# Kernel tuning notes

Measured on AMD Instinct MI355X. Metric: run time of the kernel, lower is better.

The kernel has to match this reference:

```python
import jax, jax.numpy as jnp
import numpy as np

B, L, D = 8, 2048, 64
EPS = 1e-8


def setup_inputs() -> dict:
    key = jax.random.key(0)
    ks = jax.random.split(key, 7)
    s = 1.0 / np.sqrt(D)  # ~ torch Linear default init scale
    return {
        "x": jax.random.normal(ks[0], (B, L, D), dtype=jnp.float32),
        "B_w": jax.random.normal(ks[1], (D, D), dtype=jnp.float32) * s,
        "B_b": jax.random.normal(ks[2], (D,), dtype=jnp.float32) * s,
        "C_w": jax.random.normal(ks[3], (D, D), dtype=jnp.float32) * s,
        "C_b": jax.random.normal(ks[4], (D,), dtype=jnp.float32) * s,
        "V_w": jax.random.normal(ks[5], (D, D), dtype=jnp.float32) * s,
        "V_b": jax.random.normal(ks[6], (D,), dtype=jnp.float32) * s,
    }


def reference(x, B_w, B_b, C_w, C_b, V_w, V_b):
    # torch nn.Linear: y = x @ W.T + b
    BZ = jnp.einsum('bld,ed->ble', x, B_w) + B_b   # (B,L,D)
    CZ = jnp.einsum('bld,ed->ble', x, C_w) + C_b   # (B,L,D)
    scores = jnp.einsum('bld,bmd->blm', BZ, CZ)     # (B,L,L)
    attn = jax.nn.relu(scores)
    # note: normalization over dim=-2 (column sums), as in the original
    attn = attn / (attn.sum(axis=-2, keepdims=True) + EPS)
    VZ = jnp.einsum('bld,ed->ble', x, V_w) + V_b   # (B,L,D)
    out = jnp.einsum('blm,bmd->bld', attn, VZ)      # (B,L,D)
    return x + out
```

## Files before the change

kernel.cpp:

```cpp
#include <hip/hip_runtime.h>

typedef unsigned short u16;
typedef unsigned int u32;
typedef __bf16 bf16x8 __attribute__((ext_vector_type(8)));
typedef float f32x16 __attribute__((ext_vector_type(16)));
typedef const void __attribute__((address_space(1))) gvoid;
typedef void __attribute__((address_space(3))) lvoid;

#define GLOAD16(gp, lp) __builtin_amdgcn_global_load_lds((gvoid*)(gp), (lvoid*)(lp), 16, 0, 0)
#define POST_BARRIER_FENCE() do { __builtin_amdgcn_sched_barrier(0); asm volatile("" ::: "memory"); } while (0)

namespace {
constexpr int Ln = 2048;
constexpr float EPS = 1e-8f;
}

__device__ __forceinline__ u32 pk2(float lo, float hi) {
    u32 r;
    asm("v_cvt_pk_bf16_f32 %0, %1, %2" : "=v"(r) : "v"(lo), "v"(hi));
    return r;
}

__device__ __forceinline__ void half_swap(u32 a, u32 b, u32& na, u32& nb) {
    u32 sa = (u32)__shfl_xor((int)a, 32, 64);
    u32 sb = (u32)__shfl_xor((int)b, 32, 64);
    int hi = (threadIdx.x & 63) >> 5;
    na = hi ? a : sb;
    nb = hi ? sa : b;
}

__global__ __launch_bounds__(128) void proj_k(
    const float* __restrict__ x,
    const float* __restrict__ Bw, const float* __restrict__ Bb,
    const float* __restrict__ Cw, const float* __restrict__ Cb,
    const float* __restrict__ Vw, const float* __restrict__ Vb,
    u16* __restrict__ BZh, u16* __restrict__ CZh, u16* __restrict__ VZTh)
{
    const int tid = threadIdx.x;
    const int ln = tid & 31;
    const int g5 = (tid >> 5) & 1;
    const int w  = tid >> 6;
    const int row0 = blockIdx.x * 64 + w * 32;
    const int b   = row0 >> 11;
    const int l0b = row0 & 2047;

    bf16x8 wf[3][2][4];
    const float* const Wp[3] = {Bw, Cw, Vw};
    #pragma unroll
    for (int m = 0; m < 3; ++m)
      #pragma unroll
      for (int e = 0; e < 2; ++e)
        #pragma unroll
        for (int c = 0; c < 4; ++c) {
            const float* p = Wp[m] + (e * 32 + ln) * 64 + c * 16 + g5 * 8;
            const float4 lo = *(const float4*)p;
            const float4 hi = *(const float4*)(p + 4);
            uint4 t4;
            t4.x = pk2(lo.x, lo.y); t4.y = pk2(lo.z, lo.w);
            t4.z = pk2(hi.x, hi.y); t4.w = pk2(hi.z, hi.w);
            wf[m][e][c] = __builtin_bit_cast(bf16x8, t4);
        }
    bf16x8 xf[4];
    {
        const float* xp = x + (row0 + ln) * 64 + g5 * 8;
        #pragma unroll
        for (int c = 0; c < 4; ++c) {
            const float4 lo = *(const float4*)(xp + c * 16);
            const float4 hi = *(const float4*)(xp + c * 16 + 4);
            uint4 t4;
            t4.x = pk2(lo.x, lo.y); t4.y = pk2(lo.z, lo.w);
            t4.z = pk2(hi.x, hi.y); t4.w = pk2(hi.z, hi.w);
            xf[c] = __builtin_bit_cast(bf16x8, t4);
        }
    }
    const float* const biasBC[2] = {Bb, Cb};
    u16* const outBC[2] = {BZh, CZh};
    #pragma unroll
    for (int m = 0; m < 2; ++m) {
        #pragma unroll
        for (int e = 0; e < 2; ++e) {
            f32x16 st;
            #pragma unroll
            for (int q = 0; q < 4; ++q) {
                const float4 bv = *(const float4*)(biasBC[m] + e * 32 + q * 8 + g5 * 4);
                st[q*4+0] = bv.x; st[q*4+1] = bv.y; st[q*4+2] = bv.z; st[q*4+3] = bv.w;
            }
            #pragma unroll
            for (int c = 0; c < 4; ++c)
                st = __builtin_amdgcn_mfma_f32_32x32x16_bf16(wf[m][e][c], xf[c], st, 0, 0, 0);
            u16* op = outBC[m] + (row0 + ln) * 64 + e * 32 + g5 * 4;
            #pragma unroll
            for (int q = 0; q < 4; ++q) {
                uint2 pk;
                pk.x = pk2(st[q*4+0], st[q*4+1]);
                pk.y = pk2(st[q*4+2], st[q*4+3]);
                *(uint2*)(op + q * 8) = pk;
            }
        }
    }
    #pragma unroll
    for (int e = 0; e < 2; ++e) {
        const float vb = Vb[e * 32 + ln];
        f32x16 st;
        #pragma unroll
        for (int r = 0; r < 16; ++r) st[r] = vb;
        #pragma unroll
        for (int c = 0; c < 4; ++c)
            st = __builtin_amdgcn_mfma_f32_32x32x16_bf16(xf[c], wf[2][e][c], st, 0, 0, 0);
        u16* op = VZTh + (b * 64 + e * 32 + ln) * Ln + l0b + g5 * 4;
        #pragma unroll
        for (int q = 0; q < 4; ++q) {
            uint2 pk;
            pk.x = pk2(st[q*4+0], st[q*4+1]);
            pk.y = pk2(st[q*4+2], st[q*4+3]);
            *(uint2*)(op + q * 8) = pk;
        }
    }
}

__global__ __launch_bounds__(512) void denom_k(
    const u16* __restrict__ BZh, const u16* __restrict__ CZh,
    float* __restrict__ denp)
{
    __shared__ __attribute__((aligned(16))) char smem2[65536 + 1536];
    float (*red)[5] = (float(*)[5])(smem2 + 65536);
    const int tid = threadIdx.x;
    const int lane = tid & 63;
    const int ln = lane & 31;
    const int g5 = lane >> 5;
    const int w = tid >> 6;
    const int wm2 = w & 1, wl4 = w >> 1;
    const int flat = (int)blockIdx.z * 256 + (int)blockIdx.y * 32 + (int)blockIdx.x;
    const int nf = (flat & 7) * 64 + (flat >> 3);
    const int b = nf >> 6;
    const int rem = nf & 63;
    const int mb = (rem & 31) * 64;
    const int half = rem >> 5;
    const int l0w = half * 1024 + wl4 * 256;
    char* const bufw = smem2 + w * 8192;

    bf16x8 af[4];
    {
        const u16* cp = CZh + ((b * Ln + mb + wm2 * 32 + ln) << 6) + g5 * 8;
        #pragma unroll
        for (int c = 0; c < 4; ++c) af[c] = *(const bf16x8*)(cp + c * 16);
    }
    asm volatile("s_waitcnt vmcnt(0)" ::: "memory");
    POST_BARRIER_FENCE();

    auto stageW = [&](int c) {
        const int base = b * Ln + l0w + c * 32;
        #pragma unroll
        for (int it = 0; it < 4; ++it) {
            int r = it * 8 + (lane >> 3);
            int u = (lane & 7) ^ (r & 7);
            GLOAD16(BZh + ((base + r) << 6) + (u << 3),
                    bufw + (c & 1) * 4096 + it * 1024);
        }
    };
    stageW(0); stageW(1);

    float accs[16];
    #pragma unroll
    for (int r = 0; r < 16; ++r) accs[r] = 0.f;
    #pragma unroll 1
    for (int c = 0; c < 8; ++c) {
        asm volatile("s_waitcnt vmcnt(4)" ::: "memory");
        POST_BARRIER_FENCE();
        const char* bc = bufw + (c & 1) * 4096;
        bf16x8 bfr[4];
        #pragma unroll
        for (int c2 = 0; c2 < 4; ++c2) {
            int un = (c2 << 1) | g5;
            bfr[c2] = *(const bf16x8*)(bc + (ln << 7) + ((un ^ (ln & 7)) << 4));
        }
        asm volatile("s_waitcnt lgkmcnt(0)" ::: "memory");
        POST_BARRIER_FENCE();
        if (c + 2 < 8) stageW(c + 2);
        f32x16 st = {};
        __builtin_amdgcn_s_setprio(1);
        #pragma unroll
        for (int c2 = 0; c2 < 4; ++c2)
            st = __builtin_amdgcn_mfma_f32_32x32x16_bf16(af[c2], bfr[c2], st, 0, 0, 0);
        __builtin_amdgcn_s_setprio(0);
        #pragma unroll
        for (int r = 0; r < 16; ++r) accs[r] += fmaxf(st[r], 0.f);
    }
    #pragma unroll
    for (int msk = 1; msk <= 16; msk <<= 1)
        #pragma unroll
        for (int r = 0; r < 16; ++r)
            accs[r] += __shfl_xor(accs[r], msk, 64);
    if (ln == 0) {
        #pragma unroll
        for (int r = 0; r < 16; ++r) {
            const int moff = (r & 3) + ((r >> 2) << 3) + g5 * 4;
            red[wm2 * 32 + moff][wl4] = accs[r];
        }
    }
    __syncthreads();
    if (tid < 64)
        denp[(half * 8 + b) * Ln + mb + tid] =
            red[tid][0] + red[tid][1] + red[tid][2] + red[tid][3];
}

__global__ __launch_bounds__(512, 4) void fused_out(
    const float* __restrict__ x,
    const u16* __restrict__ BZh, const u16* __restrict__ CZh,
    const u16* __restrict__ VZTh, const float* __restrict__ denp,
    float* __restrict__ out)
{
    __shared__ __attribute__((aligned(16))) char smem[73728];
    float* const denl = (float*)smem;
    char* const bufs = smem + 8192;
    const int tid = threadIdx.x;
    const int lane = tid & 63;
    const int ln = lane & 31;
    const int g5 = lane >> 5;
    const int w = tid >> 6;
    const int wm = w & 3;
    const int wl = w >> 2;
    const int bx = (int)blockIdx.x;
    const int nf = (bx & 7) * 32 + (bx >> 3);
    const int b = nf >> 5;
    const int l0 = (nf & 31) * 64;
    const int wave_base = tid & ~63;
    const int mA = wm * 32 + ln;

    auto stage = [&](int t) {
        char* bufc = bufs + (t & 1) * 32768;
        char* vzb = bufc + 16384;
        const int m0s = t << 7;
        #pragma unroll
        for (int it = 0; it < 2; ++it) {
            int j = (it << 9) + tid;
            int r = j >> 3;
            int u = (j & 7) ^ (r & 7);
            GLOAD16(CZh + ((b * Ln + m0s + r) << 6) + (u << 3),
                    bufc + ((it << 9) + wave_base) * 16);
        }
        #pragma unroll
        for (int it = 0; it < 2; ++it) {
            int j = (it << 9) + tid;
            int r = j >> 4;
            int u = (j & 15) ^ (r & 7);
            GLOAD16(VZTh + ((b << 6) + r) * Ln + m0s + (u << 3),
                    vzb + ((it << 9) + wave_base) * 16);
        }
    };

    stage(0);
    {
        const float4 c0 = *(const float4*)(denp + b * Ln + tid * 4);
        const float4 c1 = *(const float4*)(denp + (8 + b) * Ln + tid * 4);
        float4 dv;
        dv.x = 1.f / (c0.x + c1.x + EPS);
        dv.y = 1.f / (c0.y + c1.y + EPS);
        dv.z = 1.f / (c0.z + c1.z + EPS);
        dv.w = 1.f / (c0.w + c1.w + EPS);
        *(float4*)(denl + tid * 4) = dv;
    }
    bf16x8 bzf[4];
    {
        const u16* bp = BZh + ((b * Ln + l0 + wl * 32 + ln) << 6) + g5 * 8;
        #pragma unroll
        for (int c = 0; c < 4; ++c) bzf[c] = *(const bf16x8*)(bp + c * 16);
    }
    __syncthreads();

    f32x16 acc0 = {}, acc1 = {};
    for (int t = 0; t < 16; ++t) {
        if (t > 0) {
            asm volatile("s_waitcnt vmcnt(0)" ::: "memory");
            __builtin_amdgcn_s_barrier();
            POST_BARRIER_FENCE();
        }
        if (t + 1 < 16) stage(t + 1);
        const char* cz = bufs + (t & 1) * 32768;
        const char* vz = cz + 16384;
        f32x16 st = {};
        __builtin_amdgcn_s_setprio(1);
        #pragma unroll
        for (int c = 0; c < 4; ++c) {
            int un = (c << 1) | g5;
            bf16x8 a = *(const bf16x8*)(cz + (mA << 7) + ((un ^ (mA & 7)) << 4));
            st = __builtin_amdgcn_mfma_f32_32x32x16_bf16(a, bzf[c], st, 0, 0, 0);
        }
        __builtin_amdgcn_s_setprio(0);
        const int mq0 = (t << 7) + wm * 32;
        u32 wv[8];
        #pragma unroll
        for (int q = 0; q < 4; ++q) {
            const float4 dq = *(const float4*)(denl + mq0 + q * 8 + g5 * 4);
            float p0 = fmaxf(st[q*4+0], 0.f) * dq.x;
            float p1 = fmaxf(st[q*4+1], 0.f) * dq.y;
            float p2 = fmaxf(st[q*4+2], 0.f) * dq.z;
            float p3 = fmaxf(st[q*4+3], 0.f) * dq.w;
            wv[q*2+0] = pk2(p0, p1);
            wv[q*2+1] = pk2(p2, p3);
        }
        u32 f0w0, f0w1, f0w2, f0w3, f1w0, f1w1, f1w2, f1w3;
        half_swap(wv[2], wv[0], f0w2, f0w0);
        half_swap(wv[3], wv[1], f0w3, f0w1);
        half_swap(wv[6], wv[4], f1w2, f1w0);
        half_swap(wv[7], wv[5], f1w3, f1w1);
        bf16x8 pf0, pf1;
        { uint4 t4; t4.x=f0w0; t4.y=f0w1; t4.z=f0w2; t4.w=f0w3; pf0 = __builtin_bit_cast(bf16x8, t4); }
        { uint4 t4; t4.x=f1w0; t4.y=f1w1; t4.z=f1w2; t4.w=f1w3; pf1 = __builtin_bit_cast(bf16x8, t4); }
        const int un00 = (wm << 2) | g5;
        const int un01 = (wm << 2) | 2 | g5;
        __builtin_amdgcn_s_setprio(1);
        {
            bf16x8 av;
            av = *(const bf16x8*)(vz + (ln << 8) + ((un00 ^ (ln & 7)) << 4));
            acc0 = __builtin_amdgcn_mfma_f32_32x32x16_bf16(av, pf0, acc0, 0, 0, 0);
            av = *(const bf16x8*)(vz + (ln << 8) + ((un01 ^ (ln & 7)) << 4));
            acc0 = __builtin_amdgcn_mfma_f32_32x32x16_bf16(av, pf1, acc0, 0, 0, 0);
            av = *(const bf16x8*)(vz + ((32 + ln) << 8) + ((un00 ^ (ln & 7)) << 4));
            acc1 = __builtin_amdgcn_mfma_f32_32x32x16_bf16(av, pf0, acc1, 0, 0, 0);
            av = *(const bf16x8*)(vz + ((32 + ln) << 8) + ((un01 ^ (ln & 7)) << 4));
            acc1 = __builtin_amdgcn_mfma_f32_32x32x16_bf16(av, pf1, acc1, 0, 0, 0);
        }
        __builtin_amdgcn_s_setprio(0);
    }

    __syncthreads();
    float* red = (float*)bufs;
    constexpr int LSTR = 36;
    constexpr int SSTR = 64 * LSTR;
    if (wm >= 2) {
        float* base = red + (wl * 2 + (wm - 2)) * SSTR + lane * LSTR;
        #pragma unroll
        for (int r = 0; r < 16; ++r) { base[r] = acc0[r]; base[16 + r] = acc1[r]; }
    }
    __syncthreads();
    if (wm < 2) {
        float* base = red + (wl * 2 + wm) * SSTR + lane * LSTR;
        #pragma unroll
        for (int r = 0; r < 16; ++r) { acc0[r] += base[r]; acc1[r] += base[16 + r]; }
    }
    __syncthreads();
    if (wm == 1) {
        float* base = red + (4 + wl) * SSTR + lane * LSTR;
        #pragma unroll
        for (int r = 0; r < 16; ++r) { base[r] = acc0[r]; base[16 + r] = acc1[r]; }
    }
    __syncthreads();
    if (wm == 0) {
        float* base = red + (4 + wl) * SSTR + lane * LSTR;
        #pragma unroll
        for (int r = 0; r < 16; ++r) { acc0[r] += base[r]; acc1[r] += base[16 + r]; }
        const int row = b * Ln + l0 + wl * 32 + ln;
        #pragma unroll
        for (int q = 0; q < 4; ++q) {
            const int d0 = q * 8 + g5 * 4;
            const float4 x0 = *(const float4*)(x + row * 64 + d0);
            float4 o0;
            o0.x = x0.x + acc0[q*4+0]; o0.y = x0.y + acc0[q*4+1];
            o0.z = x0.z + acc0[q*4+2]; o0.w = x0.w + acc0[q*4+3];
            *(float4*)(out + row * 64 + d0) = o0;
            const float4 x1 = *(const float4*)(x + row * 64 + 32 + d0);
            float4 o1;
            o1.x = x1.x + acc1[q*4+0]; o1.y = x1.y + acc1[q*4+1];
            o1.z = x1.z + acc1[q*4+2]; o1.w = x1.w + acc1[q*4+3];
            *(float4*)(out + row * 64 + 32 + d0) = o1;
        }
    }
}

extern "C" void kernel_launch(void* const* d_in, const int* in_sizes, int n_in,
                              void* d_out, int out_size, void* d_ws, size_t ws_size,
                              hipStream_t stream) {
    const float* x  = (const float*)d_in[0];
    const float* Bw = (const float*)d_in[1];
    const float* Bb = (const float*)d_in[2];
    const float* Cw = (const float*)d_in[3];
    const float* Cb = (const float*)d_in[4];
    const float* Vw = (const float*)d_in[5];
    const float* Vb = (const float*)d_in[6];
    float* out = (float*)d_out;
    char* wsb = (char*)d_ws;
    u16* BZh  = (u16*)wsb;
    u16* CZh  = (u16*)(wsb + (2u << 20));
    u16* VZTh = (u16*)(wsb + (4u << 20));
    float* denp = (float*)(wsb + (6u << 20));

    proj_k<<<dim3(256), 128, 0, stream>>>(x, Bw, Bb, Cw, Cb, Vw, Vb, BZh, CZh, VZTh);
    denom_k<<<dim3(32, 8, 2), 512, 0, stream>>>(BZh, CZh, denp);
    fused_out<<<dim3(256), 512, 0, stream>>>(x, BZh, CZh, VZTh, denp, out);
}
```

Before: 47.05 us.

## Split fused_out into 512 blocks of 4 waves, each covering 32 rows

fused_out previously ran 256 blocks of 8 waves, with each block covering 64 query rows as two 32-row groups. It now runs 512 blocks of 4 waves, each covering 32 rows, so the work spreads over more blocks. The cross-wave reduction shrinks to a single stage of three partial sums. The cost is that each block stages the full CZ/VZ tiles for only half as many rows, doubling K/V global loads. The 72KB shared allocation per block also limits how many blocks fit per CU.

New measurement: 47.28 us. Within noise of the previous version (+0.5%).

```diff
diff --git a/kernel.cpp b/kernel.cpp
--- a/kernel.cpp
+++ b/kernel.cpp
@@ -204,7 +204,7 @@
             red[tid][0] + red[tid][1] + red[tid][2] + red[tid][3];
 }
 
-__global__ __launch_bounds__(512, 4) void fused_out(
+__global__ __launch_bounds__(256, 2) void fused_out(
     const float* __restrict__ x,
     const u16* __restrict__ BZh, const u16* __restrict__ CZh,
     const u16* __restrict__ VZTh, const float* __restrict__ denp,
@@ -217,13 +217,11 @@
     const int lane = tid & 63;
     const int ln = lane & 31;
     const int g5 = lane >> 5;
-    const int w = tid >> 6;
-    const int wm = w & 3;
-    const int wl = w >> 2;
+    const int wm = tid >> 6;
     const int bx = (int)blockIdx.x;
-    const int nf = (bx & 7) * 32 + (bx >> 3);
-    const int b = nf >> 5;
-    const int l0 = (nf & 31) * 64;
+    const int nf = (bx & 7) * 64 + (bx >> 3);
+    const int b = nf >> 6;
+    const int l0 = (nf & 63) * 32;
     const int wave_base = tid & ~63;
     const int mA = wm * 32 + ln;
 
@@ -232,37 +230,39 @@
         char* vzb = bufc + 16384;
         const int m0s = t << 7;
         #pragma unroll
-        for (int it = 0; it < 2; ++it) {
-            int j = (it << 9) + tid;
+        for (int it = 0; it < 4; ++it) {
+            int j = (it << 8) + tid;
             int r = j >> 3;
             int u = (j & 7) ^ (r & 7);
             GLOAD16(CZh + ((b * Ln + m0s + r) << 6) + (u << 3),
-                    bufc + ((it << 9) + wave_base) * 16);
-        }
-        #pragma unroll
-        for (int it = 0; it < 2; ++it) {
-            int j = (it << 9) + tid;
+                    bufc + ((it << 8) + wave_base) * 16);
+        }
+        #pragma unroll
+        for (int it = 0; it < 4; ++it) {
+            int j = (it << 8) + tid;
             int r = j >> 4;
             int u = (j & 15) ^ (r & 7);
             GLOAD16(VZTh + ((b << 6) + r) * Ln + m0s + (u << 3),
-                    vzb + ((it << 9) + wave_base) * 16);
+                    vzb + ((it << 8) + wave_base) * 16);
         }
     };
 
     stage(0);
-    {
-        const float4 c0 = *(const float4*)(denp + b * Ln + tid * 4);
-        const float4 c1 = *(const float4*)(denp + (8 + b) * Ln + tid * 4);
+    #pragma unroll
+    for (int k = 0; k < 2; ++k) {
+        const int idx = tid * 4 + k * 1024;
+        const float4 c0 = *(const float4*)(denp + b * Ln + idx);
+        const float4 c1 = *(const float4*)(denp + (8 + b) * Ln + idx);
         float4 dv;
         dv.x = 1.f / (c0.x + c1.x + EPS);
         dv.y = 1.f / (c0.y + c1.y + EPS);
         dv.z = 1.f / (c0.z + c1.z + EPS);
         dv.w = 1.f / (c0.w + c1.w + EPS);
-        *(float4*)(denl + tid * 4) = dv;
+        *(float4*)(denl + idx) = dv;
     }
     bf16x8 bzf[4];
     {
-        const u16* bp = BZh + ((b * Ln + l0 + wl * 32 + ln) << 6) + g5 * 8;
+        const u16* bp = BZh + ((b * Ln + l0 + ln) << 6) + g5 * 8;
         #pragma unroll
         for (int c = 0; c < 4; ++c) bzf[c] = *(const bf16x8*)(bp + c * 16);
     }
@@ -328,29 +328,20 @@
     float* red = (float*)bufs;
     constexpr int LSTR = 36;
     constexpr int SSTR = 64 * LSTR;
-    if (wm >= 2) {
-        float* base = red + (wl * 2 + (wm - 2)) * SSTR + lane * LSTR;
-        #pragma unroll
-        for (int r = 0; r < 16; ++r) { base[r] = acc0[r]; base[16 + r] = acc1[r]; }
-    }
-    __syncthreads();
-    if (wm < 2) {
-        float* base = red + (wl * 2 + wm) * SSTR + lane * LSTR;
-        #pragma unroll
-        for (int r = 0; r < 16; ++r) { acc0[r] += base[r]; acc1[r] += base[16 + r]; }
-    }
-    __syncthreads();
-    if (wm == 1) {
-        float* base = red + (4 + wl) * SSTR + lane * LSTR;
+    if (wm != 0) {
+        float* base = red + (wm - 1) * SSTR + lane * LSTR;
         #pragma unroll
         for (int r = 0; r < 16; ++r) { base[r] = acc0[r]; base[16 + r] = acc1[r]; }
     }
     __syncthreads();
     if (wm == 0) {
-        float* base = red + (4 + wl) * SSTR + lane * LSTR;
-        #pragma unroll
-        for (int r = 0; r < 16; ++r) { acc0[r] += base[r]; acc1[r] += base[16 + r]; }
-        const int row = b * Ln + l0 + wl * 32 + ln;
+        #pragma unroll
+        for (int s = 0; s < 3; ++s) {
+            float* base = red + s * SSTR + lane * LSTR;
+            #pragma unroll
+            for (int r = 0; r < 16; ++r) { acc0[r] += base[r]; acc1[r] += base[16 + r]; }
+        }
+        const int row = b * Ln + l0 + ln;
         #pragma unroll
         for (int q = 0; q < 4; ++q) {
             const int d0 = q * 8 + g5 * 4;
@@ -387,5 +378,5 @@
 
     proj_k<<<dim3(256), 128, 0, stream>>>(x, Bw, Bb, Cw, Cb, Vw, Vb, BZh, CZh, VZTh);
     denom_k<<<dim3(32, 8, 2), 512, 0, stream>>>(BZh, CZh, denp);
-    fused_out<<<dim3(256), 512, 0, stream>>>(x, BZh, CZh, VZTh, denp, out);
-}
+    fused_out<<<dim3(512), 256, 0, stream>>>(x, BZh, CZh, VZTh, denp, out);
+}
```
